# Optimization experiments

Hardware: AMD Instinct MI355X
Metric: run time of the kernel (lower is better)

## Reference

```python
import jax, jax.numpy as jnp
import numpy as np

H_DIM = 128; N_HEADS = 4; D_K = 32; W_INP = 300
N_DOC = 32000; N_TOPIC = 800; N_WORD = 80000; B = 16
VOCAB = 15000; N_TOPIC_EMB = 50
SQRT_DK = float(np.sqrt(D_K))


def setup_inputs() -> dict:
    key = jax.random.key(0)
    ks = iter(jax.random.split(key, 64))
    def nrm(shape, s=0.05):
        return jax.random.normal(next(ks), shape, dtype=jnp.float32) * s
    def ridx(shape, hi):
        return jax.random.randint(next(ks), shape, 0, hi, dtype=jnp.int32)
    inp = {
        'word_embeds': nrm((VOCAB, W_INP), 0.1),
        'topic_embeds': nrm((N_TOPIC_EMB, H_DIM), 0.1),
        'KW': nrm((2, 3, H_DIM, H_DIM)), 'Kb': nrm((2, 3, H_DIM)),
        'QW': nrm((2, 3, H_DIM, H_DIM)), 'Qb': nrm((2, 3, H_DIM)),
        'VW': nrm((2, 3, H_DIM, H_DIM)), 'Vb': nrm((2, 3, H_DIM)),
        'AW': nrm((2, 3, H_DIM, H_DIM)), 'Ab': nrm((2, 3, H_DIM)),
        'rel_att': nrm((2, 5, N_HEADS, D_K, D_K), 0.1),
        'rel_msg': nrm((2, 5, N_HEADS, D_K, D_K), 0.1),
        'rel_pri': jnp.ones((2, 5, N_HEADS), jnp.float32),
        'skip': jnp.ones((2, 3), jnp.float32),
        'adapt_w': nrm((W_INP, H_DIM)), 'adapt_b': nrm((H_DIM,)),
        'out_w': nrm((H_DIM, 1)), 'out_b': nrm((1,)),
        'y_data': jax.random.uniform(next(ks), (B,), dtype=jnp.float32),
        'word_ids': ridx((N_WORD,), VOCAB),
        'topic_ids': ridx((N_TOPIC,), N_TOPIC_EMB),
        'doc_gid': jnp.sort(ridx((N_DOC,), B)),
        'td_src': ridx((80000,), N_TOPIC), 'td_dst': ridx((80000,), N_DOC),
        'tt_src': ridx((20000,), N_TOPIC), 'tt_dst': ridx((20000,), N_TOPIC),
        'wd_src': ridx((250000,), N_WORD), 'wd_dst': ridx((250000,), N_DOC),
        'wt_src': ridx((100000,), N_WORD), 'wt_dst': ridx((100000,), N_TOPIC),
        'ww_src': ridx((400000,), N_WORD), 'ww_dst': ridx((400000,), N_WORD),
    }
    return inp


def _seg_attn(att, val, dst, n):
    # per-dst-node softmax over incoming edges (per head), then weighted scatter-sum
    m = jax.ops.segment_max(att, dst, num_segments=n)          # [n, H]
    m = jnp.where(jnp.isfinite(m), m, 0.0)                     # empty mailboxes -> 0
    e = jnp.exp(att - m[dst])                                  # [E, H]
    s = jax.ops.segment_sum(e, dst, num_segments=n)            # [n, H]
    w = e / jnp.where(s[dst] > 0, s[dst], 1.0)                 # [E, H]
    return jax.ops.segment_sum(w[:, :, None] * val, dst, num_segments=n)  # [n, H, dk]


def _proj(h, W, b):
    return (h @ W + b).reshape(-1, N_HEADS, D_K)


def _forward(word_embeds, topic_embeds, KW, Kb, QW, Qb, VW, Vb, AW, Ab,
             rel_att, rel_msg, rel_pri, skip, adapt_w, adapt_b, out_w, out_b,
             y_data, word_ids, topic_ids, doc_gid,
             td_src, td_dst, tt_src, tt_dst, wd_src, wd_dst,
             wt_src, wt_dst, ww_src, ww_dst):
    # node-type ids: doc=0, topic=1, word=2; etype ids: td=0 tt=1 wd=2 wt=3 ww=4
    hw = jnp.tanh(word_embeds[word_ids] @ adapt_w + adapt_b)   # [Nw, H_DIM]
    ht = topic_embeds[topic_ids]                               # [Nt, H_DIM]
    hd = jnp.zeros((N_DOC, H_DIM), dtype=word_embeds.dtype)

    def layer(hd, ht, hw, li):
        q_d = _proj(hd, QW[li, 0], Qb[li, 0])
        q_t = _proj(ht, QW[li, 1], Qb[li, 1])
        q_w = _proj(hw, QW[li, 2], Qb[li, 2])
        k_t = _proj(ht, KW[li, 1], Kb[li, 1]); v_t = _proj(ht, VW[li, 1], Vb[li, 1])
        k_w = _proj(hw, KW[li, 2], Kb[li, 2]); v_w = _proj(hw, VW[li, 2], Vb[li, 2])

        def et(k, v, q, src, dst, r, n_dst):
            ke = jnp.einsum('ehd,hdf->ehf', k[src], rel_att[li, r])
            att = (q[dst] * ke).sum(-1) * rel_pri[li, r] / SQRT_DK   # [E, H]
            val = jnp.einsum('ehd,hdf->ehf', v[src], rel_msg[li, r])
            return _seg_attn(att, val, dst, n_dst)

        # cross_reducer='mean' over etypes targeting each node type
        t_d = (et(k_t, v_t, q_d, td_src, td_dst, 0, N_DOC) +
               et(k_w, v_w, q_d, wd_src, wd_dst, 2, N_DOC)) * 0.5
        t_t = (et(k_t, v_t, q_t, tt_src, tt_dst, 1, N_TOPIC) +
               et(k_w, v_w, q_t, wt_src, wt_dst, 3, N_TOPIC)) * 0.5
        t_w = et(k_w, v_w, q_w, ww_src, ww_dst, 4, N_WORD)

        def comb(t, h, nid):
            a = jax.nn.sigmoid(skip[li, nid])
            tr = t.reshape(-1, H_DIM) @ AW[li, nid] + Ab[li, nid]
            return tr * a + h * (1.0 - a)

        return comb(t_d, hd, 0), comb(t_t, ht, 1), comb(t_w, hw, 2)

    for li in range(2):
        hd, ht, hw = layer(hd, ht, hw, li)

    g = jax.ops.segment_max(hd, doc_gid, num_segments=B)       # dgl.max_nodes over docs
    logits = (g @ out_w + out_b).reshape(-1)                   # [B]
    loss = jnp.mean(-(y_data * jax.nn.log_sigmoid(logits) +
                      (1.0 - y_data) * jax.nn.log_sigmoid(-logits)))
    return loss, jax.nn.sigmoid(logits)[:, None]


def reference(word_embeds, topic_embeds, KW, Kb, QW, Qb, VW, Vb, AW, Ab,
              rel_att, rel_msg, rel_pri, skip, adapt_w, adapt_b, out_w, out_b,
              y_data, word_ids, topic_ids, doc_gid,
              td_src, td_dst, tt_src, tt_dst, wd_src, wd_dst,
              wt_src, wt_dst, ww_src, ww_dst):
    return _forward(word_embeds, topic_embeds, KW, Kb, QW, Qb, VW, Vb, AW, Ab,
                    rel_att, rel_msg, rel_pri, skip, adapt_w, adapt_b, out_w, out_b,
                    y_data, word_ids, topic_ids, doc_gid,
                    td_src, td_dst, tt_src, tt_dst, wd_src, wd_dst,
                    wt_src, wt_dst, ww_src, ww_dst)
```

## Files before the change

kernel.cpp:

```cpp
#include <hip/hip_runtime.h>
#include <cstdint>
#include <cstddef>

#define H_DIM 128
#define N_DOC 32000
#define N_TOPIC 800
#define N_WORD 80000
#define BATCH 16
#define VOCAB 15000
#define NODES_ALL 145600
#define EDGES_ALL 850000
#define NBLK_SCAN 143
#define N4_SCAN 36400
#define LDSW 136

typedef short bf16x8 __attribute__((ext_vector_type(8)));
typedef float f32x4 __attribute__((ext_vector_type(4)));
typedef float f32x2 __attribute__((ext_vector_type(2)));
typedef unsigned short u16;
typedef unsigned char u8;

static __device__ __forceinline__ u16 f2bf(float x) {
  unsigned u = __float_as_uint(x);
  u += 0x7fffu + ((u >> 16) & 1u);
// ... 106 lines not shown
    const u16* lds16, int rr, int cs, u8* kv, size_t m, int vhalf)
{
  u8* Cp = kv + m * 256 + (cs >> 3) * 16 + (vhalf ? 8 : 0);
  #pragma unroll
  for (int q2 = 0; q2 < 4; ++q2) {
    uint4 ld = *reinterpret_cast<const uint4*>(&lds16[rr * LDSW + cs + q2 * 8]);
    int t0 = __builtin_amdgcn_cvt_pk_fp8_f32(b2f(ld.x & 0xffffu), b2f(ld.x >> 16), 0, false);
    unsigned w0 = (unsigned)__builtin_amdgcn_cvt_pk_fp8_f32(b2f(ld.y & 0xffffu), b2f(ld.y >> 16), t0, true);
    int t1 = __builtin_amdgcn_cvt_pk_fp8_f32(b2f(ld.z & 0xffffu), b2f(ld.z >> 16), 0, false);
    unsigned w1 = (unsigned)__builtin_amdgcn_cvt_pk_fp8_f32(b2f(ld.w & 0xffffu), b2f(ld.w >> 16), t1, true);
    *reinterpret_cast<uint2*>(Cp + q2 * 16) = make_uint2(w0, w1);
  }
}

static __device__ __forceinline__ void bf16_write_row(
    const u16* lds16, int rr, int cs, u16* C, size_t m)
{
  u16* Cp = C + m * 128 + cs;
  #pragma unroll
  for (int q2 = 0; q2 < 4; ++q2)
    *reinterpret_cast<uint4*>(Cp + q2 * 8) =
        *reinterpret_cast<const uint4*>(&lds16[rr * LDSW + cs + q2 * 8]);
}

#define GEMM_ACC(AV, BLP)                                                        \
  {                                                                              \
    const u16* Bp = (BLP) + (size_t)lane * 8;                                    \
    _Pragma("unroll")                                                            \
    for (int s = 0; s < 4; ++s) {                                                \
      _Pragma("unroll")                                                          \
      for (int t = 0; t < 8; ++t) {                                              \
        bf16x8 bfr = *reinterpret_cast<const bf16x8*>(Bp + (size_t)(t * 4 + s) * 512); \
        acc[t] = __builtin_amdgcn_mfma_f32_16x16x32_bf16(AV[s], bfr, acc[t], 0, 0, 0); \
      }                                                                          \
    }                                                                            \
  }

#define ACC_TO_LDS(BIAS)                                                         \
  {                                                                              \
    _Pragma("unroll")                                                            \
    for (int t = 0; t < 8; ++t) {                                                \
      const int col = t * 16 + (lane & 15);                                      \
      const float bb = (BIAS)[col];                                              \
      const int mr = w * 16 + g * 4;                                             \
      _Pragma("unroll")                                                          \
      for (int j = 0; j < 4; ++j)                                                \
        lds16[(mr + j) * LDSW + col] = f2bf(acc[t][j] + bb);                     \
    }                                                                            \
  }

static __device__ __forceinline__ float lds_qc_dot(
    const u16* lds16, int rr, int cs, const float* __restrict__ qc)
{
  float dot = 0.f;
  #pragma unroll
  for (int q2 = 0; q2 < 4; ++q2) {
    uint4 ld = *reinterpret_cast<const uint4*>(&lds16[rr * LDSW + cs + q2 * 8]);
    float4 qa = *reinterpret_cast<const float4*>(&qc[cs + q2 * 8]);
    float4 qb = *reinterpret_cast<const float4*>(&qc[cs + q2 * 8 + 4]);
    dot += b2f(ld.x & 0xffffu) * qa.x + b2f(ld.x >> 16) * qa.y
         + b2f(ld.y & 0xffffu) * qa.z + b2f(ld.y >> 16) * qa.w
         + b2f(ld.z & 0xffffu) * qb.x + b2f(ld.z >> 16) * qb.y
         + b2f(ld.w & 0xffffu) * qb.z + b2f(ld.w >> 16) * qb.w;
  }
  return dot;
}

static __device__ __forceinline__ void vp_write(
    const u16* lds16, int rr, int cs, float u_keep, u8* vp, size_t m)
{
  unsigned wpk[8];
  #pragma unroll
  for (int q2 = 0; q2 < 4; ++q2) {
    uint4 ld = *reinterpret_cast<const uint4*>(&lds16[rr * LDSW + cs + q2 * 8]);
    int t0 = __builtin_amdgcn_cvt_pk_fp8_f32(u_keep * b2f(ld.x & 0xffffu), u_keep * b2f(ld.x >> 16), 0, false);
    wpk[2 * q2] = (unsigned)__builtin_amdgcn_cvt_pk_fp8_f32(u_keep * b2f(ld.y & 0xffffu), u_keep * b2f(ld.y >> 16), t0, true);
    int t1 = __builtin_amdgcn_cvt_pk_fp8_f32(u_keep * b2f(ld.z & 0xffffu), u_keep * b2f(ld.z >> 16), 0, false);
    wpk[2 * q2 + 1] = (unsigned)__builtin_amdgcn_cvt_pk_fp8_f32(u_keep * b2f(ld.w & 0xffffu), u_keep * b2f(ld.w >> 16), t1, true);
  }
  *reinterpret_cast<uint4*>(vp + m * 128 + cs)      = make_uint4(wpk[0], wpk[1], wpk[2], wpk[3]);
  *reinterpret_cast<uint4*>(vp + m * 128 + cs + 16) = make_uint4(wpk[4], wpk[5], wpk[6], wpk[7]);
}

__global__ __launch_bounds__(256) void adapt_l0w_kernel(
    const u16* __restrict__ wtab, const int* __restrict__ word_ids,
    const u16* __restrict__ BLa, const float* __restrict__ ba,
    const u16* __restrict__ BLk, const float* __restrict__ bk,
    const u16* __restrict__ BLv, const float* __restrict__ bv,
    const u16* __restrict__ BLq, const float* __restrict__ bq,
    const float* __restrict__ qc, const float* __restrict__ priw,
    u16* __restrict__ hw, u8* __restrict__ kv, u8* __restrict__ vp,
    float* __restrict__ uf, u16* __restrict__ qout, int n)
{
  __shared__ u16 lds16[64 * LDSW];
  const int tid = threadIdx.x, lane = tid & 63, w = tid >> 6;
  int rl = blockIdx.x * 64 + w * 16 + (lane & 15);
  if (rl >= n) rl = n - 1;
  const int row = word_ids[rl];
  const int g = lane >> 4;

  bf16x8 a10[10];
  const u16* Ap = wtab + (size_t)row * 320 + g * 8;
  #pragma unroll
  for (int s = 0; s < 10; ++s) a10[s] = *reinterpret_cast<const bf16x8*>(Ap + s * 32);

  const int rr = w * 16 + (lane >> 2), cs = (lane & 3) * 32;
  const int m = blockIdx.x * 64 + rr;

  f32x4 acc[8];
  #pragma unroll
  for (int t = 0; t < 8; ++t) acc[t] = (f32x4)0.f;
  {
    const u16* Bp = BLa + (size_t)lane * 8;
    #pragma unroll
    for (int s = 0; s < 10; ++s) {
      #pragma unroll
      for (int t = 0; t < 8; ++t) {
        bf16x8 bfr = *reinterpret_cast<const bf16x8*>(Bp + (size_t)(t * 10 + s) * 512);
        acc[t] = __builtin_amdgcn_mfma_f32_16x16x32_bf16(a10[s], bfr, acc[t], 0, 0, 0);
      }
    }
  }
  #pragma unroll
  for (int t = 0; t < 8; ++t) {
    const int col = t * 16 + (lane & 15);
    const float bb = ba[col];
    const int mr = w * 16 + g * 4;
    #pragma unroll
    for (int j = 0; j < 4; ++j)
      lds16[(mr + j) * LDSW + col] = f2bf(tanhf(acc[t][j] + bb));
  }
  if (m < n) bf16_write_row(lds16, rr, cs, hw, m);
  bf16x8 an[4];
  {
    const int rloc = w * 16 + (lane & 15);
    #pragma unroll
    for (int s = 0; s < 4; ++s)
      an[s] = *reinterpret_cast<const bf16x8*>(&lds16[rloc * LDSW + s * 32 + g * 8]);
  }

  #pragma unroll
  for (int t = 0; t < 8; ++t) acc[t] = (f32x4)0.f;
  GEMM_ACC(an, BLk)
  ACC_TO_LDS(bk)
  float u_keep = 0.f;
  if (m < n) {
    kv_write_half(lds16, rr, cs, kv, m, 0);
    float dot = lds_qc_dot(lds16, rr, cs, qc);
    u_keep = __expf(dot * (priw[cs >> 5] * 0.17677669529663687f));
    uf[m * 4 + (cs >> 5)] = u_keep;
  }
  #pragma unroll
  for (int t = 0; t < 8; ++t) acc[t] = (f32x4)0.f;
  GEMM_ACC(an, BLv)
  ACC_TO_LDS(bv)
  if (m < n) {
    kv_write_half(lds16, rr, cs, kv, m, 1);
    vp_write(lds16, rr, cs, u_keep, vp, m);
  }
  #pragma unroll
  for (int t = 0; t < 8; ++t) acc[t] = (f32x4)0.f;
  GEMM_ACC(an, BLq)
  ACC_TO_LDS(bq)
  if (m < n) bf16_write_row(lds16, rr, cs, qout, m);
}

__global__ __launch_bounds__(256) void gemm_kv_kernel(
    const u16* __restrict__ A,
    const u16* __restrict__ BLk, const float* __restrict__ bk,
    const u16* __restrict__ BLv, const float* __restrict__ bv,
    u8* __restrict__ kv, int n)
{
  __shared__ u16 lds16[64 * LDSW];
  const int tid = threadIdx.x, lane = tid & 63, w = tid >> 6;
  int rl = blockIdx.x * 64 + w * 16 + (lane & 15);
  if (rl >= n) rl = n - 1;
  const int g = lane >> 4;
  bf16x8 a[4];
  const u16* Ap = A + (size_t)rl * 128 + g * 8;
  #pragma unroll
  for (int s = 0; s < 4; ++s) a[s] = *reinterpret_cast<const bf16x8*>(Ap + s * 32);
  const int rr = w * 16 + (lane >> 2), cs = (lane & 3) * 32;
  const int m = blockIdx.x * 64 + rr;

  f32x4 acc[8];
  #pragma unroll
  for (int t = 0; t < 8; ++t) acc[t] = (f32x4)0.f;
  GEMM_ACC(a, BLk)
  ACC_TO_LDS(bk)
  if (m < n) kv_write_half(lds16, rr, cs, kv, m, 0);

  #pragma unroll
  for (int t = 0; t < 8; ++t) acc[t] = (f32x4)0.f;
  GEMM_ACC(a, BLv)
  ACC_TO_LDS(bv)
  if (m < n) kv_write_half(lds16, rr, cs, kv, m, 1);
}

__global__ __launch_bounds__(256) void gemmN_l0t_kernel(
    const u16* __restrict__ A,
    const u16* __restrict__ BLk, const float* __restrict__ bk,
    const u16* __restrict__ BLv, const float* __restrict__ bv,
    const u16* __restrict__ BLq0, const float* __restrict__ bq0,
    const u16* __restrict__ BLq1, const float* __restrict__ bq1,
    const float* __restrict__ qc, const float* __restrict__ prit,
    u8* __restrict__ kv, u8* __restrict__ vp, float* __restrict__ uf,
    u16* __restrict__ q0, u16* __restrict__ q1, int n)
{
  __shared__ u16 lds16[64 * LDSW];
  const int tid = threadIdx.x, lane = tid & 63, w = tid >> 6;
  int rl = blockIdx.x * 64 + w * 16 + (lane & 15);
  if (rl >= n) rl = n - 1;
  const int g = lane >> 4;
  bf16x8 a[4];
  const u16* Ap = A + (size_t)rl * 128 + g * 8;
  #pragma unroll
  for (int s = 0; s < 4; ++s) a[s] = *reinterpret_cast<const bf16x8*>(Ap + s * 32);
  const int rr = w * 16 + (lane >> 2), cs = (lane & 3) * 32;
  const int m = blockIdx.x * 64 + rr;

  f32x4 acc[8];
  #pragma unroll
  for (int t = 0; t < 8; ++t) acc[t] = (f32x4)0.f;
  GEMM_ACC(a, BLk)
  ACC_TO_LDS(bk)
  float u_keep = 0.f;
  if (m < n) {
    kv_write_half(lds16, rr, cs, kv, m, 0);
    float dot = lds_qc_dot(lds16, rr, cs, qc);
    u_keep = __expf(dot * (prit[cs >> 5] * 0.17677669529663687f));
    uf[m * 4 + (cs >> 5)] = u_keep;
  }
  #pragma unroll
  for (int t = 0; t < 8; ++t) acc[t] = (f32x4)0.f;
  GEMM_ACC(a, BLv)
  ACC_TO_LDS(bv)
  if (m < n) {
    kv_write_half(lds16, rr, cs, kv, m, 1);
    vp_write(lds16, rr, cs, u_keep, vp, m);
  }
  #pragma unroll
  for (int t = 0; t < 8; ++t) acc[t] = (f32x4)0.f;
  GEMM_ACC(a, BLq0)
  ACC_TO_LDS(bq0)
  if (m < n) bf16_write_row(lds16, rr, cs, q0, m);

  #pragma unroll
  for (int t = 0; t < 8; ++t) acc[t] = (f32x4)0.f;
  GEMM_ACC(a, BLq1)
  ACC_TO_LDS(bq1)
  if (m < n) bf16_write_row(lds16, rr, cs, q1, m);
}

template<int KS>
__global__ __launch_bounds__(256) void gemm2_kernel(
    const u16* __restrict__ A2, const u16* __restrict__ BL0, const u16* __restrict__ BL1,
    const float* __restrict__ bias, u16* __restrict__ C,
    const float* __restrict__ skipp, int n)
{
  __shared__ u16 lds16[64 * LDSW];
  const int tid = threadIdx.x, lane = tid & 63, w = tid >> 6;
  int rl = blockIdx.x * 64 + w * 16 + (lane & 15);
  if (rl >= n) rl = n - 1;
  const int g = lane >> 4;

  bf16x8 a0[KS], a1[KS];
  const u16* Ap = A2 + (size_t)rl * 256 + g * 8;
  #pragma unroll
  for (int s = 0; s < KS; ++s) {
    a0[s] = *reinterpret_cast<const bf16x8*>(Ap + s * 32);
    a1[s] = *reinterpret_cast<const bf16x8*>(Ap + 128 + s * 32);
  }
  f32x4 acc[8];
  #pragma unroll
  for (int t = 0; t < 8; ++t) acc[t] = (f32x4)0.f;
  const u16* Bp0 = BL0 + (size_t)lane * 8;
  const u16* Bp1 = BL1 + (size_t)lane * 8;
  #pragma unroll
  for (int s = 0; s < KS; ++s) {
    #pragma unroll
    for (int t = 0; t < 8; ++t) {
      bf16x8 b0 = *reinterpret_cast<const bf16x8*>(Bp0 + (size_t)(t * KS + s) * 512);
      acc[t] = __builtin_amdgcn_mfma_f32_16x16x32_bf16(a0[s], b0, acc[t], 0, 0, 0);
      bf16x8 b1 = *reinterpret_cast<const bf16x8*>(Bp1 + (size_t)(t * KS + s) * 512);
      acc[t] = __builtin_amdgcn_mfma_f32_16x16x32_bf16(a1[s], b1, acc[t], 0, 0, 0);
    }
  }
  ACC_TO_LDS(bias)
  const int rr = w * 16 + (lane >> 2), cs = (lane & 3) * 32;
  const int m = blockIdx.x * 64 + rr;
  if (m < n) {
    const float aa = 1.f / (1.f + __expf(-skipp[0]));
    #pragma unroll
    for (int q2 = 0; q2 < 4; ++q2) {
      uint4 pr = *reinterpret_cast<const uint4*>(&lds16[rr * LDSW + cs + q2 * 8]);
      uint4 blv = *reinterpret_cast<const uint4*>(C + (size_t)m * 128 + cs + q2 * 8);
      uint4 st;
      st.x = blend2(pr.x, blv.x, aa);
      st.y = blend2(pr.y, blv.y, aa);
      st.z = blend2(pr.z, blv.z, aa);
      st.w = blend2(pr.w, blv.w, aa);
      *reinterpret_cast<uint4*>(C + (size_t)m * 128 + cs + q2 * 8) = st;
    }
  }
}

__global__ __launch_bounds__(256) void comb_dq_kernel(
    const u16* __restrict__ A2, const u16* __restrict__ BL0, const u16* __restrict__ BL1,
    const float* __restrict__ bias, const float* __restrict__ skipp,
    const u16* __restrict__ BLq0, const float* __restrict__ bq0,
    const u16* __restrict__ BLq1, const float* __restrict__ bq1,
    u16* __restrict__ hd, u16* __restrict__ q0, u16* __restrict__ q1, int n)
{
  __shared__ u16 lds16[64 * LDSW];
  const int tid = threadIdx.x, lane = tid & 63, w = tid >> 6;
  int rl = blockIdx.x * 64 + w * 16 + (lane & 15);
  if (rl >= n) rl = n - 1;
  const int g = lane >> 4;

  bf16x8 a0[4], a1[4];
  const u16* Ap = A2 + (size_t)rl * 256 + g * 8;
  #pragma unroll
  for (int s = 0; s < 4; ++s) {
    a0[s] = *reinterpret_cast<const bf16x8*>(Ap + s * 32);
    a1[s] = *reinterpret_cast<const bf16x8*>(Ap + 128 + s * 32);
  }
  f32x4 acc[8];
  #pragma unroll
  for (int t = 0; t < 8; ++t) acc[t] = (f32x4)0.f;
  {
    const u16* Bp0 = BL0 + (size_t)lane * 8;
    const u16* Bp1 = BL1 + (size_t)lane * 8;
    #pragma unroll
    for (int s = 0; s < 4; ++s) {
      #pragma unroll
      for (int t = 0; t < 8; ++t) {
        bf16x8 b0 = *reinterpret_cast<const bf16x8*>(Bp0 + (size_t)(t * 4 + s) * 512);
        acc[t] = __builtin_amdgcn_mfma_f32_16x16x32_bf16(a0[s], b0, acc[t], 0, 0, 0);
        bf16x8 b1 = *reinterpret_cast<const bf16x8*>(Bp1 + (size_t)(t * 4 + s) * 512);
        acc[t] = __builtin_amdgcn_mfma_f32_16x16x32_bf16(a1[s], b1, acc[t], 0, 0, 0);
      }
    }
  }
  const float aa = 1.f / (1.f + __expf(-skipp[0]));
  #pragma unroll
  for (int t = 0; t < 8; ++t) {
    const int col = t * 16 + (lane & 15);
    const float bb = bias[col];
    const int mr = w * 16 + g * 4;
    #pragma unroll
    for (int j = 0; j < 4; ++j)
      lds16[(mr + j) * LDSW + col] = f2bf((acc[t][j] + bb) * aa);
  }
  const int rr = w * 16 + (lane >> 2), cs = (lane & 3) * 32;
  const int m = blockIdx.x * 64 + rr;
  if (m < n) bf16_write_row(lds16, rr, cs, hd, m);
  bf16x8 an[4];
  {
    const int rloc = w * 16 + (lane & 15);
    #pragma unroll
    for (int s = 0; s < 4; ++s)
      an[s] = *reinterpret_cast<const bf16x8*>(&lds16[rloc * LDSW + s * 32 + g * 8]);
  }
  #pragma unroll
  for (int t = 0; t < 8; ++t) acc[t] = (f32x4)0.f;
  GEMM_ACC(an, BLq0)
  ACC_TO_LDS(bq0)
  if (m < n) bf16_write_row(lds16, rr, cs, q0, m);
  #pragma unroll
  for (int t = 0; t < 8; ++t) acc[t] = (f32x4)0.f;
  GEMM_ACC(an, BLq1)
  ACC_TO_LDS(bq1)
  if (m < n) bf16_write_row(lds16, rr, cs, q1, m);
}

__global__ __launch_bounds__(256) void comb_kv_kernel(
    const u16* __restrict__ Aw, const u16* __restrict__ hwold,
    const u16* __restrict__ BLc, const float* __restrict__ bc,
    const u16* __restrict__ BLk, const float* __restrict__ bk,
    const u16* __restrict__ BLv, const float* __restrict__ bv,
    const float* __restrict__ skipp, u8* __restrict__ kv, int n)
{
  __shared__ u16 lds16[64 * LDSW];
  const int tid = threadIdx.x, lane = tid & 63, w = tid >> 6;
  int rl = blockIdx.x * 64 + w * 16 + (lane & 15);
  if (rl >= n) rl = n - 1;
  const int g = lane >> 4;

  bf16x8 a[4];
  const u16* Ap = Aw + (size_t)rl * 128 + g * 8;
  #pragma unroll
  for (int s = 0; s < 4; ++s) a[s] = *reinterpret_cast<const bf16x8*>(Ap + s * 32);

  f32x4 acc[8];
  #pragma unroll
  for (int t = 0; t < 8; ++t) acc[t] = (f32x4)0.f;
  GEMM_ACC(a, BLc)
  ACC_TO_LDS(bc)
  const int rr = w * 16 + (lane >> 2), cs = (lane & 3) * 32;
  const int m = blockIdx.x * 64 + rr;
  if (m < n) {
    const float aa = 1.f / (1.f + __expf(-skipp[0]));
    #pragma unroll
    for (int q2 = 0; q2 < 4; ++q2) {
      uint4 pr = *reinterpret_cast<const uint4*>(&lds16[rr * LDSW + cs + q2 * 8]);
      uint4 blv = *reinterpret_cast<const uint4*>(hwold + (size_t)m * 128 + cs + q2 * 8);
      uint4 st;
      st.x = blend2(pr.x, blv.x, aa);
      st.y = blend2(pr.y, blv.y, aa);
      st.z = blend2(pr.z, blv.z, aa);
      st.w = blend2(pr.w, blv.w, aa);
      *reinterpret_cast<uint4*>(&lds16[rr * LDSW + cs + q2 * 8]) = st;
    }
  }
  bf16x8 an[4];
  {
    const int rloc = w * 16 + (lane & 15);
    #pragma unroll
    for (int s = 0; s < 4; ++s)
      an[s] = *reinterpret_cast<const bf16x8*>(&lds16[rloc * LDSW + s * 32 + g * 8]);
  }
  #pragma unroll
  for (int t = 0; t < 8; ++t) acc[t] = (f32x4)0.f;
  GEMM_ACC(an, BLk)
  ACC_TO_LDS(bk)
  if (m < n) kv_write_half(lds16, rr, cs, kv, m, 0);
  #pragma unroll
  for (int t = 0; t < 8; ++t) acc[t] = (f32x4)0.f;
  GEMM_ACC(an, BLv)
  ACC_TO_LDS(bv)
  if (m < n) kv_write_half(lds16, rr, cs, kv, m, 1);
}

__global__ void conv_wtab_kernel(const float* __restrict__ we, u16* __restrict__ wt) {
  int i = blockIdx.x * 256 + threadIdx.x;
  if (i < VOCAB * 320) {
    int r = i / 320, c = i - r * 320;
    wt[i] = (c < 300) ? f2bf(we[(size_t)r * 300 + c]) : (u16)0;
  }
}

__global__ void gather_topic_kernel(const float* __restrict__ emb, const int* __restrict__ ids,
                                    u16* __restrict__ out) {
  int i = blockIdx.x * 256 + threadIdx.x;
  if (i < N_TOPIC * 128) {
    int node = i >> 7, c = i & 127;
    out[i] = f2bf(emb[(size_t)ids[node] * 128 + c]);
  }
}

__global__ void count_rank_kernel(const int* __restrict__ td, const int* __restrict__ wd,
                                  const int* __restrict__ tt, const int* __restrict__ wt,
                                  const int* __restrict__ ww, int* cnt, int* __restrict__ rank) {
  int i = blockIdx.x * 256 + threadIdx.x;
  if (i >= EDGES_ALL) return;
  int b;
  if (i < 80000)       b = td[i];
  else if (i < 330000) b = 32000 + wd[i - 80000];
  else if (i < 350000) b = 64000 + tt[i - 330000];
  else if (i < 450000) b = 64800 + wt[i - 350000];
  else                 b = 65600 + ww[i - 450000];
  rank[i] = atomicAdd(&cnt[b], 1);
}

__global__ void fill_rank_kernel(const int* __restrict__ td_s, const int* __restrict__ td_d,
                                 const int* __restrict__ wd_s, const int* __restrict__ wd_d,
                                 const int* __restrict__ tt_s, const int* __restrict__ tt_d,
                                 const int* __restrict__ wt_s, const int* __restrict__ wt_d,
                                 const int* __restrict__ ww_s, const int* __restrict__ ww_d,
                                 const int* __restrict__ offs, const int* __restrict__ rank,
                                 int* __restrict__ csrc) {
  int i = blockIdx.x * 256 + threadIdx.x;
  if (i >= EDGES_ALL) return;
  int b, s;
  if (i < 80000)       { b = td_d[i];                  s = td_s[i]; }
  else if (i < 330000) { b = 32000 + wd_d[i - 80000];  s = wd_s[i - 80000]; }
  else if (i < 350000) { b = 64000 + tt_d[i - 330000]; s = tt_s[i - 330000]; }
  else if (i < 450000) { b = 64800 + wt_d[i - 350000]; s = wt_s[i - 350000]; }
  else                 { b = 65600 + ww_d[i - 450000]; s = ww_s[i - 450000]; }
  csrc[offs[b] + rank[i]] = s;
}

__global__ __launch_bounds__(256) void scanA_kernel(const int* __restrict__ cnt, int* __restrict__ bsum) {
  const int tid = threadIdx.x, lane = tid & 63, wv = tid >> 6;
  const int i4 = blockIdx.x * 256 + tid;
  int4 v = make_int4(0, 0, 0, 0);
  if (i4 < N4_SCAN) v = reinterpret_cast<const int4*>(cnt)[i4];
  int s = v.x + v.y + v.z + v.w;
  #pragma unroll
  for (int d = 1; d < 64; d <<= 1) s += __shfl_xor(s, d);
  __shared__ int ws[4];
  if (lane == 0) ws[wv] = s;
  __syncthreads();
  if (tid == 0) bsum[blockIdx.x] = ws[0] + ws[1] + ws[2] + ws[3];
}

__global__ __launch_bounds__(256) void scanB_kernel(const int* __restrict__ bsum,
                                                    int* __restrict__ bpre, int* __restrict__ offs,
                                                    unsigned* __restrict__ g) {
  const int tid = threadIdx.x, lane = tid & 63, wv = tid >> 6;
// ... 130 lines not shown
      const int eA = base + sub, eB = base + 4 + sub;
      const bool vA = eA < e1, vB = eB < e1;
      const int sA = csrc[vA ? eA : last];
      const int sB = csrc[vB ? eB : last];
      uint2 cA = *reinterpret_cast<const uint2*>(vp + (size_t)sA * 128 + sl * 8);
      uint2 cB = *reinterpret_cast<const uint2*>(vp + (size_t)sB * 128 + sl * 8);
      float uA = uf[sA * 4 + h];
      float uB = uf[sB * 4 + h];
      if (!vA) { cA = make_uint2(0u, 0u); uA = 0.f; }
      if (!vB) { cB = make_uint2(0u, 0u); uB = 0.f; }
      ss += uA + uB;
      acc0 += cvt8<false>((int)cA.x); acc1 += cvt8<true>((int)cA.x);
      acc2 += cvt8<false>((int)cA.y); acc3 += cvt8<true>((int)cA.y);
      acc0 += cvt8<false>((int)cB.x); acc1 += cvt8<true>((int)cB.x);
      acc2 += cvt8<false>((int)cB.y); acc3 += cvt8<true>((int)cB.y);
    }
  }
  butterfly4(acc0, acc1, acc2, acc3, ss, lane, red, ss_out);
}

static __device__ __forceinline__ int chbase_of(int lane) {
  return (lane & 15) * 8 + ((lane >> 4) & 1) * 4 + ((lane >> 5) & 1) * 2;
}

template<int DOCU>
__global__ __launch_bounds__(256) void agg_all_kernel(AggArgs A, int topic_n)
{
  __shared__ float lacc[4][128];
  __shared__ float lssA[4];
  const int tid = threadIdx.x, lane = tid & 63, wv = tid >> 6;
  const int sub = lane >> 4, sl = lane & 15;
  const int bid = blockIdx.x;
  const int chb = chbase_of(lane);
  f32x2 red; float ss;

  if (bid < topic_n) {
    const int node = bid;
    for (int r = 0; r < 2; ++r) {
      agg_core(r ? A.q_wt : A.q_tt, r ? A.kv_w : A.kv_t,
               A.offs + (r ? 64800 : 64000), A.csrc, A.pri + (r ? 12 : 4),
               node, wv * 4 + sub, 16, sl, lane, red, ss);
      lacc[wv][chb] = red[0]; lacc[wv][chb + 1] = red[1];
      if (lane == 0) lssA[wv] = ss;
      __syncthreads();
      if (tid < 128) {
        float a = lacc[0][tid] + lacc[1][tid] + lacc[2][tid] + lacc[3][tid];
        float st = lssA[0] + lssA[1] + lssA[2] + lssA[3];
        float inv = (st > 0.f) ? 1.f / st : 0.f;
        A.t2_t[(size_t)node * 256 + r * 128 + tid] = f2bf(a * inv);
      }
      __syncthreads();
    }
  } else if (bid < topic_n + 8000) {
    const int node = (bid - topic_n) * 4 + wv;
    if (DOCU) {
      agg_docu(A.vp_t, A.uf_t, A.offs + 0, A.csrc, node, sub, sl, lane, red, ss);
    } else {
      agg_core(A.q_td, A.kv_t, A.offs + 0, A.csrc, A.pri + 0, node, sub, 4, sl, lane, red, ss);
    }
    {
      float inv = (ss > 0.f) ? 1.f / ss : 0.f;
      unsigned pk = (unsigned)f2bf(red[0] * inv) | ((unsigned)f2bf(red[1] * inv) << 16);
      *reinterpret_cast<unsigned*>(A.t2_d + (size_t)node * 256 + chb) = pk;
    }
    if (DOCU) {
      agg_docu(A.vp_w, A.uf_w, A.offs + 32000, A.csrc, node, sub, sl, lane, red, ss);
    } else {
      agg_core(A.q_wd, A.kv_w, A.offs + 32000, A.csrc, A.pri + 8, node, sub, 4, sl, lane, red, ss);
    }
    {
      float inv = (ss > 0.f) ? 1.f / ss : 0.f;
      unsigned pk = (unsigned)f2bf(red[0] * inv) | ((unsigned)f2bf(red[1] * inv) << 16);
      *reinterpret_cast<unsigned*>(A.t2_d + (size_t)node * 256 + 128 + chb) = pk;
    }
  } else {
    const int node = (bid - topic_n - 8000) * 4 + wv;
    agg_core(A.q_ww, A.kv_w, A.offs + 65600, A.csrc, A.pri + 16, node, sub, 4, sl, lane, red, ss);
    float inv = (ss > 0.f) ? 1.f / ss : 0.f;
    unsigned pk = (unsigned)f2bf(red[0] * inv) | ((unsigned)f2bf(red[1] * inv) << 16);
    *reinterpret_cast<unsigned*>(A.t_w + (size_t)node * 128 + chb) = pk;
  }
}

__global__ void segmax_kernel(const u16* __restrict__ hd, const int* __restrict__ gid,
                              unsigned* g) {
  int c = threadIdx.x;
  int d0 = blockIdx.x * 128;
  int dend = min(d0 + 128, N_DOC);
  int cur = -1; float m = 0.f;
  for (int d = d0; d < dend; ++d) {
    int gg = gid[d];
    float v = b2f(hd[(size_t)d * 128 + c]);
    if (gg != cur) {
      if (cur >= 0) atomicMax(&g[cur * 128 + c], fenc(m));
      cur = gg; m = v;
    } else {
      m = fmaxf(m, v);
    }
  }
  if (cur >= 0) atomicMax(&g[cur * 128 + c], fenc(m));
}

__global__ void final_kernel(const unsigned* __restrict__ g, const float* __restrict__ out_w,
                             const float* __restrict__ out_b, const float* __restrict__ y,
                             float* out) {
  int tid = threadIdx.x;
  int b = tid >> 4, seg = tid & 15;
  float p = 0.f;
  #pragma unroll
  for (int j = 0; j < 8; ++j) {
    int c = seg * 8 + j;
    p += fdec(g[b * 128 + c]) * out_w[c];
  }
  p += __shfl_xor(p, 1);
  p += __shfl_xor(p, 2);
  p += __shfl_xor(p, 4);
  p += __shfl_xor(p, 8);
  __shared__ float logits[BATCH];
  __shared__ float losses[BATCH];
  if (seg == 0) logits[b] = p + out_b[0];
  __syncthreads();
  if (tid < BATCH) {
    float l = logits[tid];
    out[1 + tid] = 1.f / (1.f + expf(-l));
    float ls_pos = (l > 0.f) ? -log1pf(expf(-l)) : l - log1pf(expf(l));
    float ls_neg = (l < 0.f) ? -log1pf(expf(l)) : -l - log1pf(expf(-l));
    losses[tid] = -(y[tid] * ls_pos + (1.f - y[tid]) * ls_neg);
  }
  __syncthreads();
  if (tid == 0) {
    float s = 0.f;
    for (int j = 0; j < BATCH; ++j) s += losses[j];
    out[0] = s / (float)BATCH;
  }
}

extern "C" void kernel_launch(void* const* d_in, const int* in_sizes, int n_in,
                              void* d_out, int out_size, void* d_ws, size_t ws_size,
                              hipStream_t stream)
{
  const float* word_embeds  = (const float*)d_in[0];
  const float* topic_embeds = (const float*)d_in[1];
  const float* KW  = (const float*)d_in[2];
  const float* Kb  = (const float*)d_in[3];
  const float* QW  = (const float*)d_in[4];
  const float* Qb  = (const float*)d_in[5];
  const float* VW  = (const float*)d_in[6];
  const float* Vb  = (const float*)d_in[7];
  const float* AW  = (const float*)d_in[8];
  const float* Ab  = (const float*)d_in[9];
  const float* rel_att = (const float*)d_in[10];
  const float* rel_msg = (const float*)d_in[11];
  const float* rel_pri = (const float*)d_in[12];
  const float* skip    = (const float*)d_in[13];
  const float* adapt_w = (const float*)d_in[14];
  const float* adapt_b = (const float*)d_in[15];
  const float* out_w   = (const float*)d_in[16];
  const float* out_b   = (const float*)d_in[17];
  const float* y_data  = (const float*)d_in[18];
  const int* word_ids  = (const int*)d_in[19];
  const int* topic_ids = (const int*)d_in[20];
  const int* doc_gid   = (const int*)d_in[21];
  const int* td_src = (const int*)d_in[22];
  const int* td_dst = (const int*)d_in[23];
  const int* tt_src = (const int*)d_in[24];
  const int* tt_dst = (const int*)d_in[25];
  const int* wd_src = (const int*)d_in[26];
  const int* wd_dst = (const int*)d_in[27];
  const int* wt_src = (const int*)d_in[28];
  const int* wt_dst = (const int*)d_in[29];
  const int* ww_src = (const int*)d_in[30];
  const int* ww_dst = (const int*)d_in[31];

  char* base = (char*)d_ws;
  size_t off_b = 0;
  auto alloc = [&](size_t bytes) -> char* {
    char* p = base + off_b;
    off_b = (off_b + bytes + 255) & ~(size_t)255;
    return p;
  };

  u16* wtab = (u16*)alloc((size_t)VOCAB * 320 * 2);
  u16* hw   = (u16*)alloc((size_t)N_WORD * 128 * 2);
  u16* hd   = (u16*)alloc((size_t)N_DOC * 128 * 2);
  u16* ht   = (u16*)alloc((size_t)N_TOPIC * 128 * 2);
  u8*  kv_w = (u8*)alloc((size_t)N_WORD * 256);
  u8*  kv_t = (u8*)alloc((size_t)N_TOPIC * 256);
  u8*  vp_w = (u8*)alloc((size_t)N_WORD * 128);
  u8*  vp_t = (u8*)alloc((size_t)N_TOPIC * 128);
  float* uf_w = (float*)alloc((size_t)N_WORD * 4 * 4);
  float* uf_t = (float*)alloc((size_t)N_TOPIC * 4 * 4);
  u16* q_td = (u16*)alloc((size_t)N_DOC * 128 * 2);
  u16* q_wd = (u16*)alloc((size_t)N_DOC * 128 * 2);
  u16* q_tt = (u16*)alloc((size_t)N_TOPIC * 128 * 2);
  u16* q_wt = (u16*)alloc((size_t)N_TOPIC * 128 * 2);
  u16* q_ww = (u16*)alloc((size_t)N_WORD * 128 * 2);
  u16* t2_d = (u16*)alloc((size_t)N_DOC * 256 * 2);
  u16* t2_t = (u16*)alloc((size_t)N_TOPIC * 256 * 2);
  u16* t_w  = (u16*)alloc((size_t)N_WORD * 128 * 2);
  unsigned* g = (unsigned*)alloc((size_t)BATCH * 128 * 4);

  int* cnt_all  = (int*)alloc((size_t)NODES_ALL * 4);
  int* offs_all = (int*)alloc(((size_t)NODES_ALL + 1) * 4);
  int* csrc_all = (int*)alloc((size_t)EDGES_ALL * 4);
  int* rank_all = (int*)alloc((size_t)EDGES_ALL * 4);
  int* bsum     = (int*)alloc((size_t)NBLK_SCAN * 4);
  int* bpre     = (int*)alloc((size_t)NBLK_SCAN * 4);

  u16* blw        = (u16*)alloc((size_t)(40960 + 28 * 16384) * 2);
  float* bias_are = (float*)alloc((size_t)29 * 128 * 4);

  auto BLp = [&](int wid) -> const u16* {
    return (wid == 0) ? blw : blw + 40960 + (size_t)(wid - 1) * 16384;
  };
  auto BIp = [&](int wid) -> const float* { return bias_are + wid * 128; };
  auto WID = [&](int li, int j) { return 1 + li * 14 + j; };

  prep_kernel<<<29 * 8, 256, 0, stream>>>(KW, Kb, QW, Qb, VW, Vb, AW, Ab,
                                          rel_att, rel_msg, adapt_w, adapt_b, blw, bias_are);
  conv_wtab_kernel<<<(VOCAB * 320 + 255) / 256, 256, 0, stream>>>(word_embeds, wtab);
  gather_topic_kernel<<<(N_TOPIC * 128 + 255) / 256, 256, 0, stream>>>(topic_embeds, topic_ids, ht);

  hipMemsetAsync(cnt_all, 0, (size_t)NODES_ALL * 4, stream);
  count_rank_kernel<<<(EDGES_ALL + 255) / 256, 256, 0, stream>>>(
      td_dst, wd_dst, tt_dst, wt_dst, ww_dst, cnt_all, rank_all);
  scanA_kernel<<<NBLK_SCAN, 256, 0, stream>>>(cnt_all, bsum);
  scanB_kernel<<<1, 256, 0, stream>>>(bsum, bpre, offs_all, g);
  scanC_kernel<<<NBLK_SCAN, 256, 0, stream>>>(cnt_all, bpre, offs_all);
  fill_rank_kernel<<<(EDGES_ALL + 255) / 256, 256, 0, stream>>>(
      td_src, td_dst, wd_src, wd_dst, tt_src, tt_dst, wt_src, wt_dst, ww_src, ww_dst,
      offs_all, rank_all, csrc_all);

  const int GW = (N_WORD + 63) / 64, GD = (N_DOC + 63) / 64, GT = (N_TOPIC + 63) / 64;

  adapt_l0w_kernel<<<GW, 256, 0, stream>>>(
      wtab, word_ids,
      BLp(0), BIp(0),
      BLp(WID(0, 1)), BIp(WID(0, 1)),
      BLp(WID(0, 3)), BIp(WID(0, 3)),
      BLp(WID(0, 8)), BIp(WID(0, 8)),
      BIp(WID(0, 6)), rel_pri + 8,
      hw, kv_w, vp_w, uf_w, q_ww, N_WORD);
  gemmN_l0t_kernel<<<GT, 256, 0, stream>>>(
      ht,
      BLp(WID(0, 0)), BIp(WID(0, 0)),
      BLp(WID(0, 2)), BIp(WID(0, 2)),
      BLp(WID(0, 5)), BIp(WID(0, 5)),
      BLp(WID(0, 7)), BIp(WID(0, 7)),
      BIp(WID(0, 4)), rel_pri + 0,
      kv_t, vp_t, uf_t, q_tt, q_wt, N_TOPIC);

  AggArgs A0;
  A0.q_td = q_td; A0.q_wd = q_wd; A0.q_tt = q_tt; A0.q_wt = q_wt; A0.q_ww = q_ww;
  A0.kv_t = kv_t; A0.kv_w = kv_w; A0.vp_t = vp_t; A0.vp_w = vp_w;
  A0.uf_t = uf_t; A0.uf_w = uf_w;
  A0.csrc = csrc_all; A0.offs = offs_all;
  A0.pri = rel_pri;
  A0.t2_d = t2_d; A0.t2_t = t2_t; A0.t_w = t_w;
  agg_all_kernel<1><<<28800, 256, 0, stream>>>(A0, 800);

  comb_dq_kernel<<<GD, 256, 0, stream>>>(
      t2_d, BLp(WID(0, 9)), BLp(WID(0, 11)), BIp(WID(0, 9)), skip + 0,
      BLp(WID(1, 4)), BIp(WID(1, 4)), BLp(WID(1, 6)), BIp(WID(1, 6)),
      hd, q_td, q_wd, N_DOC);
  gemm2_kernel<4><<<GT, 256, 0, stream>>>(t2_t, BLp(WID(0, 10)), BLp(WID(0, 12)),
                                          BIp(WID(0, 10)), ht, skip + 1, N_TOPIC);
  comb_kv_kernel<<<GW, 256, 0, stream>>>(
      t_w, hw, BLp(WID(0, 13)), BIp(WID(0, 13)),
      BLp(WID(1, 1)), BIp(WID(1, 1)), BLp(WID(1, 3)), BIp(WID(1, 3)),
      skip + 2, kv_w, N_WORD);

  gemm_kv_kernel<<<GT, 256, 0, stream>>>(
      ht, BLp(WID(1, 0)), BIp(WID(1, 0)), BLp(WID(1, 2)), BIp(WID(1, 2)), kv_t, N_TOPIC);

  AggArgs A1 = A0;
  A1.pri = rel_pri + 20;
  agg_all_kernel<0><<<8000, 256, 0, stream>>>(A1, 0);

  gemm2_kernel<4><<<GD, 256, 0, stream>>>(t2_d, BLp(WID(1, 9)), BLp(WID(1, 11)),
                                          BIp(WID(1, 9)), hd, skip + 3, N_DOC);

  segmax_kernel<<<(N_DOC + 127) / 128, 128, 0, stream>>>(hd, doc_gid, g);
  final_kernel<<<1, 256, 0, stream>>>(g, out_w, out_b, y_data, (float*)d_out);
}
```

Baseline: 372.8 us.

## Shrink GEMM kernels to single-wave blocks and fuse final combine with doc segmax

The per-node GEMM kernels (adapt, kv, topic, gemm2, comb_dq, comb_kv) are reshaped from 256-thread blocks of 64 rows to 64-thread single-wave blocks of 16 rows. This launches four times as many blocks, which is meant to improve load balance and occupancy. The last-layer doc combine GEMM is merged with the graph max-pooling readout into a new comb_readout kernel. That kernel does the per-group segment max from LDS with atomicMax and never writes hd back to global memory, so the separate segmax pass and its re-read of hd are gone. In exchange, B-matrix weight loads are reused across fewer rows per block, and each block in the readout issues more atomics.

```diff
diff --git a/kernel.cpp b/kernel.cpp
--- a/kernel.cpp
+++ b/kernel.cpp
@@ -212,7 +212,7 @@
   *reinterpret_cast<uint4*>(vp + m * 128 + cs + 16) = make_uint4(wpk[4], wpk[5], wpk[6], wpk[7]);
 }
 
-__global__ __launch_bounds__(256) void adapt_l0w_kernel(
+__global__ __launch_bounds__(64) void adapt_l0w_kernel(
     const u16* __restrict__ wtab, const int* __restrict__ word_ids,
     const u16* __restrict__ BLa, const float* __restrict__ ba,
     const u16* __restrict__ BLk, const float* __restrict__ bk,
@@ -222,9 +222,10 @@
     u16* __restrict__ hw, u8* __restrict__ kv, u8* __restrict__ vp,
     float* __restrict__ uf, u16* __restrict__ qout, int n)
 {
-  __shared__ u16 lds16[64 * LDSW];
-  const int tid = threadIdx.x, lane = tid & 63, w = tid >> 6;
-  int rl = blockIdx.x * 64 + w * 16 + (lane & 15);
+  __shared__ u16 lds16[16 * LDSW];
+  const int lane = threadIdx.x;
+  const int w = 0;
+  int rl = blockIdx.x * 16 + (lane & 15);
   if (rl >= n) rl = n - 1;
   const int row = word_ids[rl];
   const int g = lane >> 4;
@@ -234,8 +235,8 @@
   #pragma unroll
   for (int s = 0; s < 10; ++s) a10[s] = *reinterpret_cast<const bf16x8*>(Ap + s * 32);
 
-  const int rr = w * 16 + (lane >> 2), cs = (lane & 3) * 32;
-  const int m = blockIdx.x * 64 + rr;
+  const int rr = lane >> 2, cs = (lane & 3) * 32;
+  const int m = blockIdx.x * 16 + rr;
 
   f32x4 acc[8];
   #pragma unroll
@@ -255,7 +256,7 @@
   for (int t = 0; t < 8; ++t) {
     const int col = t * 16 + (lane & 15);
     const float bb = ba[col];
-    const int mr = w * 16 + g * 4;
+    const int mr = g * 4;
     #pragma unroll
     for (int j = 0; j < 4; ++j)
       lds16[(mr + j) * LDSW + col] = f2bf(tanhf(acc[t][j] + bb));
@@ -263,7 +264,7 @@
   if (m < n) bf16_write_row(lds16, rr, cs, hw, m);
   bf16x8 an[4];
   {
-    const int rloc = w * 16 + (lane & 15);
+    const int rloc = lane & 15;
     #pragma unroll
     for (int s = 0; s < 4; ++s)
       an[s] = *reinterpret_cast<const bf16x8*>(&lds16[rloc * LDSW + s * 32 + g * 8]);
@@ -295,23 +296,24 @@
   if (m < n) bf16_write_row(lds16, rr, cs, qout, m);
 }
 
-__global__ __launch_bounds__(256) void gemm_kv_kernel(
+__global__ __launch_bounds__(64) void gemm_kv_kernel(
     const u16* __restrict__ A,
     const u16* __restrict__ BLk, const float* __restrict__ bk,
     const u16* __restrict__ BLv, const float* __restrict__ bv,
     u8* __restrict__ kv, int n)
 {
-  __shared__ u16 lds16[64 * LDSW];
-  const int tid = threadIdx.x, lane = tid & 63, w = tid >> 6;
-  int rl = blockIdx.x * 64 + w * 16 + (lane & 15);
+  __shared__ u16 lds16[16 * LDSW];
+  const int lane = threadIdx.x;
+  const int w = 0;
+  int rl = blockIdx.x * 16 + (lane & 15);
   if (rl >= n) rl = n - 1;
   const int g = lane >> 4;
   bf16x8 a[4];
   const u16* Ap = A + (size_t)rl * 128 + g * 8;
   #pragma unroll
   for (int s = 0; s < 4; ++s) a[s] = *reinterpret_cast<const bf16x8*>(Ap + s * 32);
-  const int rr = w * 16 + (lane >> 2), cs = (lane & 3) * 32;
-  const int m = blockIdx.x * 64 + rr;
+  const int rr = lane >> 2, cs = (lane & 3) * 32;
+  const int m = blockIdx.x * 16 + rr;
 
   f32x4 acc[8];
   #pragma unroll
@@ -327,7 +329,7 @@
   if (m < n) kv_write_half(lds16, rr, cs, kv, m, 1);
 }
 
-__global__ __launch_bounds__(256) void gemmN_l0t_kernel(
+__global__ __launch_bounds__(64) void gemmN_l0t_kernel(
     const u16* __restrict__ A,
     const u16* __restrict__ BLk, const float* __restrict__ bk,
     const u16* __restrict__ BLv, const float* __restrict__ bv,
@@ -337,17 +339,18 @@
     u8* __restrict__ kv, u8* __restrict__ vp, float* __restrict__ uf,
     u16* __restrict__ q0, u16* __restrict__ q1, int n)
 {
-  __shared__ u16 lds16[64 * LDSW];
-  const int tid = threadIdx.x, lane = tid & 63, w = tid >> 6;
-  int rl = blockIdx.x * 64 + w * 16 + (lane & 15);
+  __shared__ u16 lds16[16 * LDSW];
+  const int lane = threadIdx.x;
+  const int w = 0;
+  int rl = blockIdx.x * 16 + (lane & 15);
   if (rl >= n) rl = n - 1;
   const int g = lane >> 4;
   bf16x8 a[4];
   const u16* Ap = A + (size_t)rl * 128 + g * 8;
   #pragma unroll
   for (int s = 0; s < 4; ++s) a[s] = *reinterpret_cast<const bf16x8*>(Ap + s * 32);
-  const int rr = w * 16 + (lane >> 2), cs = (lane & 3) * 32;
-  const int m = blockIdx.x * 64 + rr;
+  const int rr = lane >> 2, cs = (lane & 3) * 32;
+  const int m = blockIdx.x * 16 + rr;
 
   f32x4 acc[8];
   #pragma unroll
@@ -382,22 +385,22 @@
   if (m < n) bf16_write_row(lds16, rr, cs, q1, m);
 }
 
-template<int KS>
-__global__ __launch_bounds__(256) void gemm2_kernel(
+__global__ __launch_bounds__(64) void gemm2_kernel(
     const u16* __restrict__ A2, const u16* __restrict__ BL0, const u16* __restrict__ BL1,
     const float* __restrict__ bias, u16* __restrict__ C,
     const float* __restrict__ skipp, int n)
 {
-  __shared__ u16 lds16[64 * LDSW];
-  const int tid = threadIdx.x, lane = tid & 63, w = tid >> 6;
-  int rl = blockIdx.x * 64 + w * 16 + (lane & 15);
+  __shared__ u16 lds16[16 * LDSW];
+  const int lane = threadIdx.x;
+  const int w = 0;
+  int rl = blockIdx.x * 16 + (lane & 15);
   if (rl >= n) rl = n - 1;
   const int g = lane >> 4;
 
-  bf16x8 a0[KS], a1[KS];
+  bf16x8 a0[4], a1[4];
   const u16* Ap = A2 + (size_t)rl * 256 + g * 8;
   #pragma unroll
-  for (int s = 0; s < KS; ++s) {
+  for (int s = 0; s < 4; ++s) {
     a0[s] = *reinterpret_cast<const bf16x8*>(Ap + s * 32);
     a1[s] = *reinterpret_cast<const bf16x8*>(Ap + 128 + s * 32);
   }
@@ -407,18 +410,18 @@
   const u16* Bp0 = BL0 + (size_t)lane * 8;
   const u16* Bp1 = BL1 + (size_t)lane * 8;
   #pragma unroll
-  for (int s = 0; s < KS; ++s) {
+  for (int s = 0; s < 4; ++s) {
     #pragma unroll
     for (int t = 0; t < 8; ++t) {
-      bf16x8 b0 = *reinterpret_cast<const bf16x8*>(Bp0 + (size_t)(t * KS + s) * 512);
+      bf16x8 b0 = *reinterpret_cast<const bf16x8*>(Bp0 + (size_t)(t * 4 + s) * 512);
       acc[t] = __builtin_amdgcn_mfma_f32_16x16x32_bf16(a0[s], b0, acc[t], 0, 0, 0);
-      bf16x8 b1 = *reinterpret_cast<const bf16x8*>(Bp1 + (size_t)(t * KS + s) * 512);
+      bf16x8 b1 = *reinterpret_cast<const bf16x8*>(Bp1 + (size_t)(t * 4 + s) * 512);
       acc[t] = __builtin_amdgcn_mfma_f32_16x16x32_bf16(a1[s], b1, acc[t], 0, 0, 0);
     }
   }
   ACC_TO_LDS(bias)
-  const int rr = w * 16 + (lane >> 2), cs = (lane & 3) * 32;
-  const int m = blockIdx.x * 64 + rr;
+  const int rr = lane >> 2, cs = (lane & 3) * 32;
+  const int m = blockIdx.x * 16 + rr;
   if (m < n) {
     const float aa = 1.f / (1.f + __expf(-skipp[0]));
     #pragma unroll
@@ -435,21 +438,20 @@
   }
 }
 
-__global__ __launch_bounds__(256) void comb_dq_kernel(
+__global__ __launch_bounds__(256) void comb_readout_kernel(
     const u16* __restrict__ A2, const u16* __restrict__ BL0, const u16* __restrict__ BL1,
-    const float* __restrict__ bias, const float* __restrict__ skipp,
-    const u16* __restrict__ BLq0, const float* __restrict__ bq0,
-    const u16* __restrict__ BLq1, const float* __restrict__ bq1,
-    u16* __restrict__ hd, u16* __restrict__ q0, u16* __restrict__ q1, int n)
+    const float* __restrict__ bias, const u16* __restrict__ hdold,
+    const float* __restrict__ skipp, const int* __restrict__ gid,
+    unsigned* __restrict__ g, int n)
 {
   __shared__ u16 lds16[64 * LDSW];
   const int tid = threadIdx.x, lane = tid & 63, w = tid >> 6;
   int rl = blockIdx.x * 64 + w * 16 + (lane & 15);
   if (rl >= n) rl = n - 1;
-  const int g = lane >> 4;
+  const int gq = lane >> 4;
 
   bf16x8 a0[4], a1[4];
-  const u16* Ap = A2 + (size_t)rl * 256 + g * 8;
+  const u16* Ap = A2 + (size_t)rl * 256 + gq * 8;
   #pragma unroll
   for (int s = 0; s < 4; ++s) {
     a0[s] = *reinterpret_cast<const bf16x8*>(Ap + s * 32);
@@ -472,22 +474,104 @@
       }
     }
   }
-  const float aa = 1.f / (1.f + __expf(-skipp[0]));
   #pragma unroll
   for (int t = 0; t < 8; ++t) {
     const int col = t * 16 + (lane & 15);
     const float bb = bias[col];
-    const int mr = w * 16 + g * 4;
+    const int mr = w * 16 + gq * 4;
+    #pragma unroll
+    for (int j = 0; j < 4; ++j)
+      lds16[(mr + j) * LDSW + col] = f2bf(acc[t][j] + bb);
+  }
+  const int rr = w * 16 + (lane >> 2), cs = (lane & 3) * 32;
+  const int m = blockIdx.x * 64 + rr;
+  if (m < n) {
+    const float aa = 1.f / (1.f + __expf(-skipp[0]));
+    #pragma unroll
+    for (int q2 = 0; q2 < 4; ++q2) {
+      uint4 pr = *reinterpret_cast<const uint4*>(&lds16[rr * LDSW + cs + q2 * 8]);
+      uint4 blv = *reinterpret_cast<const uint4*>(hdold + (size_t)m * 128 + cs + q2 * 8);
+      uint4 st;
+      st.x = blend2(pr.x, blv.x, aa);
+      st.y = blend2(pr.y, blv.y, aa);
+      st.z = blend2(pr.z, blv.z, aa);
+      st.w = blend2(pr.w, blv.w, aa);
+      *reinterpret_cast<uint4*>(&lds16[rr * LDSW + cs + q2 * 8]) = st;
+    }
+  }
+  __syncthreads();
+  if (tid < 128) {
+    const int c = tid;
+    const int rmax = min(64, n - blockIdx.x * 64);
+    int cur = -1; float mx = 0.f;
+    for (int r = 0; r < rmax; ++r) {
+      int gg = gid[blockIdx.x * 64 + r];
+      float v = b2f(lds16[r * LDSW + c]);
+      if (gg != cur) {
+        if (cur >= 0) atomicMax(&g[cur * 128 + c], fenc(mx));
+        cur = gg; mx = v;
+      } else {
+        mx = fmaxf(mx, v);
+      }
+    }
+    if (cur >= 0) atomicMax(&g[cur * 128 + c], fenc(mx));
+  }
+}
+
+__global__ __launch_bounds__(64) void comb_dq_kernel(
+    const u16* __restrict__ A2, const u16* __restrict__ BL0, const u16* __restrict__ BL1,
+    const float* __restrict__ bias, const float* __restrict__ skipp,
+    const u16* __restrict__ BLq0, const float* __restrict__ bq0,
+    const u16* __restrict__ BLq1, const float* __restrict__ bq1,
+    u16* __restrict__ hd, u16* __restrict__ q0, u16* __restrict__ q1, int n)
+{
+  __shared__ u16 lds16[16 * LDSW];
+  const int lane = threadIdx.x;
+  const int w = 0;
+  int rl = blockIdx.x * 16 + (lane & 15);
+  if (rl >= n) rl = n - 1;
+  const int g = lane >> 4;
+
+  bf16x8 a0[4], a1[4];
+  const u16* Ap = A2 + (size_t)rl * 256 + g * 8;
+  #pragma unroll
+  for (int s = 0; s < 4; ++s) {
+    a0[s] = *reinterpret_cast<const bf16x8*>(Ap + s * 32);
+    a1[s] = *reinterpret_cast<const bf16x8*>(Ap + 128 + s * 32);
+  }
+  f32x4 acc[8];
+  #pragma unroll
+  for (int t = 0; t < 8; ++t) acc[t] = (f32x4)0.f;
+  {
+    const u16* Bp0 = BL0 + (size_t)lane * 8;
+    const u16* Bp1 = BL1 + (size_t)lane * 8;
+    #pragma unroll
+    for (int s = 0; s < 4; ++s) {
+      #pragma unroll
+      for (int t = 0; t < 8; ++t) {
+        bf16x8 b0 = *reinterpret_cast<const bf16x8*>(Bp0 + (size_t)(t * 4 + s) * 512);
+        acc[t] = __builtin_amdgcn_mfma_f32_16x16x32_bf16(a0[s], b0, acc[t], 0, 0, 0);
+        bf16x8 b1 = *reinterpret_cast<const bf16x8*>(Bp1 + (size_t)(t * 4 + s) * 512);
+        acc[t] = __builtin_amdgcn_mfma_f32_16x16x32_bf16(a1[s], b1, acc[t], 0, 0, 0);
+      }
+    }
+  }
+  const float aa = 1.f / (1.f + __expf(-skipp[0]));
+  #pragma unroll
+  for (int t = 0; t < 8; ++t) {
+    const int col = t * 16 + (lane & 15);
+    const float bb = bias[col];
+    const int mr = g * 4;
     #pragma unroll
     for (int j = 0; j < 4; ++j)
       lds16[(mr + j) * LDSW + col] = f2bf((acc[t][j] + bb) * aa);
   }
-  const int rr = w * 16 + (lane >> 2), cs = (lane & 3) * 32;
-  const int m = blockIdx.x * 64 + rr;
+  const int rr = lane >> 2, cs = (lane & 3) * 32;
+  const int m = blockIdx.x * 16 + rr;
   if (m < n) bf16_write_row(lds16, rr, cs, hd, m);
   bf16x8 an[4];
   {
-    const int rloc = w * 16 + (lane & 15);
+    const int rloc = lane & 15;
     #pragma unroll
     for (int s = 0; s < 4; ++s)
       an[s] = *reinterpret_cast<const bf16x8*>(&lds16[rloc * LDSW + s * 32 + g * 8]);
@@ -504,16 +588,17 @@
   if (m < n) bf16_write_row(lds16, rr, cs, q1, m);
 }
 
-__global__ __launch_bounds__(256) void comb_kv_kernel(
+__global__ __launch_bounds__(64) void comb_kv_kernel(
     const u16* __restrict__ Aw, const u16* __restrict__ hwold,
     const u16* __restrict__ BLc, const float* __restrict__ bc,
     const u16* __restrict__ BLk, const float* __restrict__ bk,
     const u16* __restrict__ BLv, const float* __restrict__ bv,
     const float* __restrict__ skipp, u8* __restrict__ kv, int n)
 {
-  __shared__ u16 lds16[64 * LDSW];
-  const int tid = threadIdx.x, lane = tid & 63, w = tid >> 6;
-  int rl = blockIdx.x * 64 + w * 16 + (lane & 15);
+  __shared__ u16 lds16[16 * LDSW];
+  const int lane = threadIdx.x;
+  const int w = 0;
+  int rl = blockIdx.x * 16 + (lane & 15);
   if (rl >= n) rl = n - 1;
   const int g = lane >> 4;
 
@@ -527,8 +612,8 @@
   for (int t = 0; t < 8; ++t) acc[t] = (f32x4)0.f;
   GEMM_ACC(a, BLc)
   ACC_TO_LDS(bc)
-  const int rr = w * 16 + (lane >> 2), cs = (lane & 3) * 32;
-  const int m = blockIdx.x * 64 + rr;
+  const int rr = lane >> 2, cs = (lane & 3) * 32;
+  const int m = blockIdx.x * 16 + rr;
   if (m < n) {
     const float aa = 1.f / (1.f + __expf(-skipp[0]));
     #pragma unroll
@@ -545,7 +630,7 @@
   }
   bf16x8 an[4];
   {
-    const int rloc = w * 16 + (lane & 15);
+    const int rloc = lane & 15;
     #pragma unroll
     for (int s = 0; s < 4; ++s)
       an[s] = *reinterpret_cast<const bf16x8*>(&lds16[rloc * LDSW + s * 32 + g * 8]);
@@ -842,25 +927,6 @@
   }
 }
 
-__global__ void segmax_kernel(const u16* __restrict__ hd, const int* __restrict__ gid,
-                              unsigned* g) {
-  int c = threadIdx.x;
-  int d0 = blockIdx.x * 128;
-  int dend = min(d0 + 128, N_DOC);
-  int cur = -1; float m = 0.f;
-  for (int d = d0; d < dend; ++d) {
-    int gg = gid[d];
-    float v = b2f(hd[(size_t)d * 128 + c]);
-    if (gg != cur) {
-      if (cur >= 0) atomicMax(&g[cur * 128 + c], fenc(m));
-      cur = gg; m = v;
-    } else {
-      m = fmaxf(m, v);
-    }
-  }
-  if (cur >= 0) atomicMax(&g[cur * 128 + c], fenc(m));
-}
-
 __global__ void final_kernel(const unsigned* __restrict__ g, const float* __restrict__ out_w,
                              const float* __restrict__ out_b, const float* __restrict__ y,
                              float* out) {
@@ -991,9 +1057,10 @@
       td_src, td_dst, wd_src, wd_dst, tt_src, tt_dst, wt_src, wt_dst, ww_src, ww_dst,
       offs_all, rank_all, csrc_all);
 
-  const int GW = (N_WORD + 63) / 64, GD = (N_DOC + 63) / 64, GT = (N_TOPIC + 63) / 64;
-
-  adapt_l0w_kernel<<<GW, 256, 0, stream>>>(
+  const int GW16 = (N_WORD + 15) / 16, GD16 = (N_DOC + 15) / 16, GT16 = (N_TOPIC + 15) / 16;
+  const int GD = (N_DOC + 63) / 64;
+
+  adapt_l0w_kernel<<<GW16, 64, 0, stream>>>(
       wtab, word_ids,
       BLp(0), BIp(0),
       BLp(WID(0, 1)), BIp(WID(0, 1)),
@@ -1001,7 +1068,7 @@
       BLp(WID(0, 8)), BIp(WID(0, 8)),
       BIp(WID(0, 6)), rel_pri + 8,
       hw, kv_w, vp_w, uf_w, q_ww, N_WORD);
-  gemmN_l0t_kernel<<<GT, 256, 0, stream>>>(
+  gemmN_l0t_kernel<<<GT16, 64, 0, stream>>>(
       ht,
       BLp(WID(0, 0)), BIp(WID(0, 0)),
       BLp(WID(0, 2)), BIp(WID(0, 2)),
@@ -1019,27 +1086,27 @@
   A0.t2_d = t2_d; A0.t2_t = t2_t; A0.t_w = t_w;
   agg_all_kernel<1><<<28800, 256, 0, stream>>>(A0, 800);
 
-  comb_dq_kernel<<<GD, 256, 0, stream>>>(
+  comb_dq_kernel<<<GD16, 64, 0, stream>>>(
       t2_d, BLp(WID(0, 9)), BLp(WID(0, 11)), BIp(WID(0, 9)), skip + 0,
       BLp(WID(1, 4)), BIp(WID(1, 4)), BLp(WID(1, 6)), BIp(WID(1, 6)),
       hd, q_td, q_wd, N_DOC);
-  gemm2_kernel<4><<<GT, 256, 0, stream>>>(t2_t, BLp(WID(0, 10)), BLp(WID(0, 12)),
-                                          BIp(WID(0, 10)), ht, skip + 1, N_TOPIC);
-  comb_kv_kernel<<<GW, 256, 0, stream>>>(
+  gemm2_kernel<<<GT16, 64, 0, stream>>>(t2_t, BLp(WID(0, 10)), BLp(WID(0, 12)),
+                                        BIp(WID(0, 10)), ht, skip + 1, N_TOPIC);
+  comb_kv_kernel<<<GW16, 64, 0, stream>>>(
       t_w, hw, BLp(WID(0, 13)), BIp(WID(0, 13)),
       BLp(WID(1, 1)), BIp(WID(1, 1)), BLp(WID(1, 3)), BIp(WID(1, 3)),
       skip + 2, kv_w, N_WORD);
 
-  gemm_kv_kernel<<<GT, 256, 0, stream>>>(
+  gemm_kv_kernel<<<GT16, 64, 0, stream>>>(
       ht, BLp(WID(1, 0)), BIp(WID(1, 0)), BLp(WID(1, 2)), BIp(WID(1, 2)), kv_t, N_TOPIC);
 
   AggArgs A1 = A0;
   A1.pri = rel_pri + 20;
   agg_all_kernel<0><<<8000, 256, 0, stream>>>(A1, 0);
 
-  gemm2_kernel<4><<<GD, 256, 0, stream>>>(t2_d, BLp(WID(1, 9)), BLp(WID(1, 11)),
-                                          BIp(WID(1, 9)), hd, skip + 3, N_DOC);
-
-  segmax_kernel<<<(N_DOC + 127) / 128, 128, 0, stream>>>(hd, doc_gid, g);
+  comb_readout_kernel<<<GD, 256, 0, stream>>>(
+      t2_d, BLp(WID(1, 9)), BLp(WID(1, 11)), BIp(WID(1, 9)), hd,
+      skip + 3, doc_gid, g, N_DOC);
+
   final_kernel<<<1, 256, 0, stream>>>(g, out_w, out_b, y_data, (float*)d_out);
 }
```

After: 335.9 us (median of 2 runs). 1.11x faster.
